# Kernel optimization log

Measured on AMD Instinct MI355X. Metric: run time of the kernel, lower is better.

## Reference

```python
import jax, jax.numpy as jnp
import numpy as np
from jax import lax

# Conv4d decomposed (as in the torch implementation) into a sum of Conv3d's
# over the first spatial kernel axis. Each 3D conv is vectorized by folding
# the strided first-dim slices into the batch dimension.

def conv4d(x, w, b, stride=(2, 2, 2, 2), padding=(1, 1, 1, 1)):
    # x: [B, Ci, D1, D2, D3, D4]; w: [Co, Ci, K1, K2, K3, K4]; b: [Co]
    B, Ci, D1, D2, D3, D4 = x.shape
    Co, _, K1, K2, K3, K4 = w.shape
    s1, p1 = stride[0], padding[0]
    T = (D1 + 2 * p1 - K1) // s1 + 1  # output size along first spatial dim
    xp = jnp.pad(x, ((0, 0), (0, 0), (p1, p1), (0, 0), (0, 0), (0, 0)))
    pad3 = [(padding[j], padding[j]) for j in (1, 2, 3)]
    out = None
    for i in range(K1):  # small fixed loop over kernel taps along dim0
        xi = xp[:, :, i:i + s1 * (T - 1) + 1:s1]           # [B, Ci, T, D2, D3, D4]
        xi = jnp.moveaxis(xi, 2, 1).reshape(B * T, Ci, D2, D3, D4)
        yi = lax.conv_general_dilated(
            xi, w[:, :, i], window_strides=stride[1:], padding=pad3,
            dimension_numbers=('NCDHW', 'OIDHW', 'NCDHW'))
        out = yi if out is None else out + yi
    O2, O3, O4 = out.shape[2], out.shape[3], out.shape[4]
    out = out.reshape(B, T, Co, O2, O3, O4)
    out = jnp.moveaxis(out, 1, 2)                          # [B, Co, T, O2, O3, O4]
    return out + b[None, :, None, None, None, None]


def setup_inputs() -> dict:
    key = jax.random.key(0)
    k0, k1, k2, k3, k4 = jax.random.split(key, 5)
    C, R = 16, 4  # in_channel, mlp_ratio
    H = C * R     # 64
    x = jax.random.normal(k0, (1, C, 32, 32, 32, 32), dtype=jnp.float32)
    w1 = jax.random.normal(k1, (H, C, 3, 3, 3, 3), dtype=jnp.float32) * 0.02
    b1 = jax.random.normal(k2, (H,), dtype=jnp.float32) * 0.02
    w2 = jax.random.normal(k3, (C, H, 3, 3, 3, 3), dtype=jnp.float32) * 0.02
    b2 = jax.random.normal(k4, (C,), dtype=jnp.float32) * 0.02
    return {'x': x, 'w1': w1, 'b1': b1, 'w2': w2, 'b2': b2}


def reference(x, w1, b1, w2, b2):
    h = conv4d(x, w1, b1)                      # [1, 64, 16, 16, 16, 16]
    h = jax.nn.gelu(h, approximate=False)      # exact erf GELU (torch default)
    return conv4d(h, w2, b2)                   # [1, 16, 8, 8, 8, 8]
```

## Files before the change

kernel.cpp:

```cpp
#include <hip/hip_runtime.h>
#include <hip/hip_bf16.h>
#include <math.h>


typedef __attribute__((ext_vector_type(8))) short short8;
typedef __attribute__((ext_vector_type(4))) float f32x4;
typedef __attribute__((ext_vector_type(4))) unsigned int uint4v;

__device__ __forceinline__ unsigned short f2bf(float v) {
    __hip_bfloat16 b = __float2bfloat16(v);
    return *(unsigned short*)&b;
}

__global__ void setup_kernel(const float* __restrict__ w1, const float* __restrict__ w2,
                             const float* __restrict__ b2,
                             unsigned short* __restrict__ w1p, unsigned short* __restrict__ w2p,
                             uint4v* __restrict__ hz, float* __restrict__ out) {
    int b = blockIdx.x, tid = threadIdx.x;
    if (b < 544) {
        int i = b * 256 + tid;
        int kp = i % 136, co = (i / 136) & 63, ci = i / 8704;
        float v = 0.f;
        if (kp < 108 && (kp & 3) < 3) v = w1[(co * 16 + ci) * 81 + (kp >> 2) * 3 + (kp & 3)];
        w1p[i] = f2bf(v);
    } else if (b < 1088) {
        int i = (b - 544) * 256 + tid;
        int kp = i % 136, co = (i / 136) & 15, ci = i / 2176;
        float v = 0.f;
        if (kp < 108 && (kp & 3) < 3) v = w2[(co * 64 + ci) * 81 + (kp >> 2) * 3 + (kp & 3)];
        w2p[i] = f2bf(v);
    } else if (b < 1344) {
        int i = (b - 1088) * 256 + tid;
        out[i] = b2[i >> 12];
    } else {
        int i = (b - 1344) * 256 + tid;
        hz[i] = (uint4v){0, 0, 0, 0};
        int j = i + 704512;
        if (j < 839808) hz[j] = (uint4v){0, 0, 0, 0};
    }
}

__global__ __launch_bounds__(256) void conv1_mfma(
        const float* __restrict__ x, const unsigned short* __restrict__ w1p,
        const float* __restrict__ b1, unsigned short* __restrict__ hpad) {
    __shared__ unsigned short sX[36000];

    const int tid = threadIdx.x;
    const int bid = blockIdx.x;
    const int t4 = bid & 1, t3 = (bid >> 1) & 7, t2 = (bid >> 4) & 7, t1 = bid >> 7;
    const int bo1 = 2 * t1, bo2 = 2 * t2, bo3 = 2 * t3, bo4 = 8 * t4;
    const int g1b = 2 * bo1 - 1, g2b = 2 * bo2 - 1, g3b = 2 * bo3 - 1, g4b = 2 * bo4 - 1;

    int offs[5], swb[5];
    unsigned mka = 0, mkb = 0;
#pragma unroll
    for (int r = 0; r < 5; ++r) {
        int u = tid + 256 * r;
        bool uok = u < 1125;
        int uu = uok ? u : 0;
        int p = uu % 9, q = uu / 9;
        int i3 = q % 5; q /= 5;
        int i2 = q % 5; int i1 = q / 5;
        int g1 = g1b + i1, g2 = g2b + i2, g3 = g3b + i3;
        bool ok123 = uok & ((unsigned)g1 < 32u) & ((unsigned)g2 < 32u) & ((unsigned)g3 < 32u);
        int g4a = g4b + 2 * p;
        offs[r] = ((g1 * 32 + g2) * 32 + g3) * 32 + g4a;
        if (ok123 && (unsigned)g4a < 32u) mka |= 1u << r;
        if (ok123 && (unsigned)(g4a + 1) < 32u) mkb |= 1u << r;
        swb[r] = 2 * (((i1 * 5 + i2) * 5 + i3) * 18 + 2 * p);
    }

    auto gatherX = [&](int ci, float (&a)[5], float (&b)[5]) {
        const float* xc = x + (size_t)ci * 1048576;
#pragma unroll
        for (int r = 0; r < 5; ++r) {
            float va = 0.f, vb = 0.f;
            if ((mka >> r) & 1) va = xc[offs[r]];
            if ((mkb >> r) & 1) vb = xc[offs[r] + 1];
            a[r] = va; b[r] = vb;
        }
    };
    auto writeSlab = [&](int ci, const float (&a)[5], const float (&b)[5]) {
        char* slab = (char*)sX + ci * 4500;
#pragma unroll
        for (int r = 0; r < 4; ++r)
            *(unsigned*)(slab + swb[r]) = (unsigned)f2bf(a[r]) | ((unsigned)f2bf(b[r]) << 16);
        if (tid < 101)
            *(unsigned*)(slab + swb[4]) = (unsigned)f2bf(a[4]) | ((unsigned)f2bf(b[4]) << 16);
    };

    {
        float a0[5], b0[5], a1[5], b1v[5];
        gatherX(0, a0, b0);
        gatherX(1, a1, b1v);
        for (int cc = 0; cc < 16; cc += 2) {
            writeSlab(cc, a0, b0);
            if (cc + 2 < 16) gatherX(cc + 2, a0, b0);
            writeSlab(cc + 1, a1, b1v);
            if (cc + 3 < 16) gatherX(cc + 3, a1, b1v);
        }
    }
    __syncthreads();

    const int lane = tid & 63, wv = tid >> 6;
    const int n16 = lane & 15, hi = lane >> 4;
    const int ct0 = 2 * (wv & 1);
    const int st0 = 2 * (wv >> 1);

    int fpb[2];
#pragma unroll
    for (int tt = 0; tt < 2; ++tt) {
        int sp = (st0 + tt) * 16 + n16;
        int o4l = sp & 7, o3l = (sp >> 3) & 1, o2l = (sp >> 4) & 1, o1l = sp >> 5;
        fpb[tt] = 2 * (900 * o1l + 180 * o2l + 36 * o3l + 2 * o4l);
    }
    int kof[4][2];
#pragma unroll
    for (int ks = 0; ks < 4; ++ks)
#pragma unroll
    for (int j = 0; j < 2; ++j) {
        int g = 8 * ks + 2 * hi + j;
        if (g > 26) g = 26;
        int k1 = g / 9, k2 = (g / 3) % 3, k3 = g % 3;
        kof[ks][j] = 2 * (450 * k1 + 90 * k2 + 18 * k3);
    }

    auto loadA = [&](int ci, short8 (&Ac)[8]) {
        const unsigned short* aw0 = w1p + (size_t)(ci * 64 + 16 * ct0 + n16) * 136 + hi * 8;
#pragma unroll
        for (int k = 0; k < 4; ++k) Ac[k] = *(const short8*)(aw0 + 32 * k);
        const unsigned short* aw1 = aw0 + 16 * 136;
#pragma unroll
        for (int k = 0; k < 4; ++k) Ac[4 + k] = *(const short8*)(aw1 + 32 * k);
    };
    auto readFR = [&](int ci, short8 (&fr)[2][4]) {
        const char* sx = (const char*)sX + ci * 4500;
#pragma unroll
        for (int tt = 0; tt < 2; ++tt) {
            const char* base = sx + fpb[tt];
#pragma unroll
            for (int ks = 0; ks < 4; ++ks) {
                unsigned r0 = *(const unsigned*)(base + kof[ks][0]);
                unsigned r1 = *(const unsigned*)(base + kof[ks][0] + 4);
                unsigned r2 = *(const unsigned*)(base + kof[ks][1]);
                unsigned r3 = *(const unsigned*)(base + kof[ks][1] + 4);
                uint4v t = (uint4v){r0, r1, r2, r3};
                fr[tt][ks] = *(short8*)&t;
            }
        }
    };

    f32x4 acc[2][2];
#pragma unroll
    for (int c = 0; c < 2; ++c)
#pragma unroll
    for (int t = 0; t < 2; ++t) acc[c][t] = (f32x4){0.f, 0.f, 0.f, 0.f};

    auto mfma16 = [&](const short8 (&Ac)[8], const short8 (&fr)[2][4]) {
        __builtin_amdgcn_s_setprio(1);
#pragma unroll
        for (int tt = 0; tt < 2; ++tt)
#pragma unroll
        for (int ks = 0; ks < 4; ++ks) {
            acc[0][tt] = __builtin_amdgcn_mfma_f32_16x16x32_bf16(Ac[ks],     fr[tt][ks], acc[0][tt], 0, 0, 0);
            acc[1][tt] = __builtin_amdgcn_mfma_f32_16x16x32_bf16(Ac[4 + ks], fr[tt][ks], acc[1][tt], 0, 0, 0);
        }
        __builtin_amdgcn_s_setprio(0);
    };

    short8 A0[8], A1[8], F0[2][4], F1[2][4];
    loadA(0, A0);
    loadA(1, A1);
    readFR(0, F0);

    for (int cc = 0; cc < 16; cc += 2) {
        readFR(cc + 1, F1);
        mfma16(A0, F0);
        if (cc < 14) { loadA(cc + 2, A0); readFR(cc + 2, F0); }
        mfma16(A1, F1);
        if (cc < 14) loadA(cc + 3, A1);
    }

#pragma unroll
    for (int c = 0; c < 2; ++c) {
#pragma unroll
        for (int tt = 0; tt < 2; ++tt) {
            int spl = 16 * (st0 + tt) + n16;
            int e4 = spl & 7, e3 = (spl >> 3) & 1, e2 = (spl >> 4) & 1, e1 = spl >> 5;
            size_t base = (size_t)(bo1 + e1 + 1) * 5832 + (bo2 + e2 + 1) * 324 +
                          (bo3 + e3 + 1) * 18 + (bo4 + e4 + 1);
#pragma unroll
            for (int r = 0; r < 4; ++r) {
                int co = 16 * (ct0 + c) + 4 * hi + r;
                float v = acc[c][tt][r] + b1[co];
                v = 0.5f * v * (1.f + erff(v * 0.70710678118654752f));
                hpad[(size_t)co * 104976 + base] = f2bf(v);
            }
        }
    }
}

__global__ __launch_bounds__(256) void conv2_mfma(
        const unsigned short* __restrict__ hpad, const unsigned short* __restrict__ w2p,
        float* __restrict__ out) {
    __shared__ unsigned short sX[18000];

    const int tid = threadIdx.x;
    const int bid = blockIdx.x;
    const int s = bid & 63, cig = bid >> 6;
    const int t3 = s & 3, t2 = (s >> 2) & 3, t1 = s >> 4;
    const int bo1 = 2 * t1, bo2 = 2 * t2, bo3 = 2 * t3;

    int offs[5], swb[5];
#pragma unroll
    for (int r = 0; r < 5; ++r) {
        int u = tid + 256 * r;
        if (u >= 1125) u = 0;
        int p = u % 9, q = u / 9;
        int i3 = q % 5; q /= 5;
        int i2 = q % 5; int i1 = q / 5;
        offs[r] = (2 * bo1 + i1) * 5832 + (2 * bo2 + i2) * 324 + (2 * bo3 + i3) * 18 + 2 * p;
        swb[r] = 2 * (((i1 * 5 + i2) * 5 + i3) * 18 + 2 * p);
    }

    {
        unsigned fa[5], na[5];
        const unsigned short* h0 = hpad + (size_t)(cig * 8) * 104976;
#pragma unroll
        for (int r = 0; r < 5; ++r) fa[r] = *(const unsigned*)(h0 + offs[r]);
        for (int s8 = 0; s8 < 8; ++s8) {
            if (s8 < 7) {
                const unsigned short* hc = hpad + (size_t)(cig * 8 + s8 + 1) * 104976;
#pragma unroll
                for (int r = 0; r < 5; ++r) na[r] = *(const unsigned*)(hc + offs[r]);
            }
            char* slab = (char*)sX + s8 * 4500;
#pragma unroll
            for (int r = 0; r < 4; ++r) *(unsigned*)(slab + swb[r]) = fa[r];
            if (tid < 101) *(unsigned*)(slab + swb[4]) = fa[4];
            if (s8 < 7) {
#pragma unroll
                for (int r = 0; r < 5; ++r) fa[r] = na[r];
            }
        }
    }
    __syncthreads();

    const int lane = tid & 63, wv = tid >> 6;
    const int n16 = lane & 15, hi = lane >> 4;

    int fpb;
    {
        int sp = wv * 16 + n16;
        int o4l = sp & 7, o3l = (sp >> 3) & 1, o2l = (sp >> 4) & 1, o1l = sp >> 5;
        fpb = 2 * (900 * o1l + 180 * o2l + 36 * o3l + 2 * o4l);
    }
    int kof[4][2];
#pragma unroll
    for (int ks = 0; ks < 4; ++ks)
#pragma unroll
    for (int j = 0; j < 2; ++j) {
        int g = 8 * ks + 2 * hi + j;
        if (g > 26) g = 26;
        int k1 = g / 9, k2 = (g / 3) % 3, k3 = g % 3;
        kof[ks][j] = 2 * (450 * k1 + 90 * k2 + 18 * k3);
    }

    auto loadA = [&](int s8, short8 (&Ac)[4]) {
        const unsigned short* aw = w2p + (size_t)((cig * 8 + s8) * 16 + n16) * 136 + hi * 8;
#pragma unroll
        for (int k = 0; k < 4; ++k) Ac[k] = *(const short8*)(aw + 32 * k);
    };
    auto readFR = [&](int s8, short8 (&fr)[4]) {
        const char* base = (const char*)sX + s8 * 4500 + fpb;
#pragma unroll
        for (int ks = 0; ks < 4; ++ks) {
            unsigned r0 = *(const unsigned*)(base + kof[ks][0]);
            unsigned r1 = *(const unsigned*)(base + kof[ks][0] + 4);
            unsigned r2 = *(const unsigned*)(base + kof[ks][1]);
            unsigned r3 = *(const unsigned*)(base + kof[ks][1] + 4);
            uint4v tmp = (uint4v){r0, r1, r2, r3};
            fr[ks] = *(short8*)&tmp;
        }
    };

    f32x4 acc = (f32x4){0.f, 0.f, 0.f, 0.f};
    short8 A0[4], A1[4], F0[4], F1[4];
    loadA(0, A0);
    loadA(1, A1);
    readFR(0, F0);

    auto mfma4 = [&](const short8 (&Ac)[4], const short8 (&fr)[4]) {
        __builtin_amdgcn_s_setprio(1);
#pragma unroll
        for (int ks = 0; ks < 4; ++ks)
            acc = __builtin_amdgcn_mfma_f32_16x16x32_bf16(Ac[ks], fr[ks], acc, 0, 0, 0);
        __builtin_amdgcn_s_setprio(0);
    };

    for (int cc = 0; cc < 8; cc += 2) {
        readFR(cc + 1, F1);
        mfma4(A0, F0);
        if (cc < 6) { loadA(cc + 2, A0); readFR(cc + 2, F0); }
        mfma4(A1, F1);
        if (cc < 6) loadA(cc + 3, A1);
    }

    {
        int spl = 16 * wv + n16;
        int e4 = spl & 7, e3 = (spl >> 3) & 1, e2 = (spl >> 4) & 1, e1 = spl >> 5;
        int o1 = bo1 + e1, o2 = bo2 + e2, o3 = bo3 + e3, o4 = e4;
#pragma unroll
        for (int r = 0; r < 4; ++r) {
            int co = 4 * hi + r;
            atomicAdd(&out[(size_t)co * 4096 + o1 * 512 + o2 * 64 + o3 * 8 + o4], acc[r]);
        }
    }
}

extern "C" void kernel_launch(void* const* d_in, const int* in_sizes, int n_in,
                              void* d_out, int out_size, void* d_ws, size_t ws_size,
                              hipStream_t stream) {
    const float* x  = (const float*)d_in[0];
    const float* w1 = (const float*)d_in[1];
    const float* b1 = (const float*)d_in[2];
    const float* w2 = (const float*)d_in[3];
    const float* b2 = (const float*)d_in[4];
    float* out = (float*)d_out;

    unsigned short* hpad = (unsigned short*)d_ws;
    unsigned short* w1p  = hpad + 6718464;
    unsigned short* w2p  = w1p + 139264;

    setup_kernel<<<4096, 256, 0, stream>>>(w1, w2, b2, w1p, w2p, (uint4v*)hpad, out);
    conv1_mfma<<<1024, 256, 0, stream>>>(x, w1p, b1, hpad);
    conv2_mfma<<<512, 256, 0, stream>>>(hpad, w2p, out);
}
```

Before: 85.98 us.

## Split conv1 tiles across eight waves and vectorize input gather

conv1_mfma now runs 512 threads per block. Each of the 8 waves computes one 16-wide spatial tile for two channel tiles, where before each of 4 waves computed two spatial tiles. The input gather fetches each pair of adjacent floats with one 8-byte load from a clamped offset, then masks the out-of-bounds values to zero, in 3 rounds instead of 5. This aims to raise wave-level parallelism and latency hiding while using fewer, wider loads. The cost is that each wave now reloads the same weight fragments, so weight traffic doubles.

```diff
diff --git a/kernel.cpp b/kernel.cpp
--- a/kernel.cpp
+++ b/kernel.cpp
@@ -6,6 +6,7 @@
 typedef __attribute__((ext_vector_type(8))) short short8;
 typedef __attribute__((ext_vector_type(4))) float f32x4;
 typedef __attribute__((ext_vector_type(4))) unsigned int uint4v;
+typedef unsigned uint2a __attribute__((ext_vector_type(2), aligned(4)));
 
 __device__ __forceinline__ unsigned short f2bf(float v) {
     __hip_bfloat16 b = __float2bfloat16(v);
@@ -40,7 +41,7 @@
     }
 }
 
-__global__ __launch_bounds__(256) void conv1_mfma(
+__global__ __launch_bounds__(512) void conv1_mfma(
         const float* __restrict__ x, const unsigned short* __restrict__ w1p,
         const float* __restrict__ b1, unsigned short* __restrict__ hpad) {
     __shared__ unsigned short sX[36000];
@@ -51,11 +52,11 @@
     const int bo1 = 2 * t1, bo2 = 2 * t2, bo3 = 2 * t3, bo4 = 8 * t4;
     const int g1b = 2 * bo1 - 1, g2b = 2 * bo2 - 1, g3b = 2 * bo3 - 1, g4b = 2 * bo4 - 1;
 
-    int offs[5], swb[5];
+    int offc[3], swb[3];
     unsigned mka = 0, mkb = 0;
 #pragma unroll
-    for (int r = 0; r < 5; ++r) {
-        int u = tid + 256 * r;
+    for (int r = 0; r < 3; ++r) {
+        int u = tid + 512 * r;
         bool uok = u < 1125;
         int uu = uok ? u : 0;
         int p = uu % 9, q = uu / 9;
@@ -64,33 +65,33 @@
         int g1 = g1b + i1, g2 = g2b + i2, g3 = g3b + i3;
         bool ok123 = uok & ((unsigned)g1 < 32u) & ((unsigned)g2 < 32u) & ((unsigned)g3 < 32u);
         int g4a = g4b + 2 * p;
-        offs[r] = ((g1 * 32 + g2) * 32 + g3) * 32 + g4a;
+        int off = ((g1 * 32 + g2) * 32 + g3) * 32 + g4a;
         if (ok123 && (unsigned)g4a < 32u) mka |= 1u << r;
         if (ok123 && (unsigned)(g4a + 1) < 32u) mkb |= 1u << r;
+        offc[r] = off < 0 ? 0 : (off > 1048574 ? 1048574 : off);
         swb[r] = 2 * (((i1 * 5 + i2) * 5 + i3) * 18 + 2 * p);
     }
 
-    auto gatherX = [&](int ci, float (&a)[5], float (&b)[5]) {
+    auto gatherX = [&](int ci, float (&a)[3], float (&b)[3]) {
         const float* xc = x + (size_t)ci * 1048576;
 #pragma unroll
-        for (int r = 0; r < 5; ++r) {
-            float va = 0.f, vb = 0.f;
-            if ((mka >> r) & 1) va = xc[offs[r]];
-            if ((mkb >> r) & 1) vb = xc[offs[r] + 1];
-            a[r] = va; b[r] = vb;
-        }
-    };
-    auto writeSlab = [&](int ci, const float (&a)[5], const float (&b)[5]) {
+        for (int r = 0; r < 3; ++r) {
+            uint2a v = *(const uint2a*)(xc + offc[r]);
+            a[r] = ((mka >> r) & 1) ? __uint_as_float(v.x) : 0.f;
+            b[r] = ((mkb >> r) & 1) ? __uint_as_float(v.y) : 0.f;
+        }
+    };
+    auto writeSlab = [&](int ci, const float (&a)[3], const float (&b)[3]) {
         char* slab = (char*)sX + ci * 4500;
 #pragma unroll
-        for (int r = 0; r < 4; ++r)
+        for (int r = 0; r < 2; ++r)
             *(unsigned*)(slab + swb[r]) = (unsigned)f2bf(a[r]) | ((unsigned)f2bf(b[r]) << 16);
         if (tid < 101)
-            *(unsigned*)(slab + swb[4]) = (unsigned)f2bf(a[4]) | ((unsigned)f2bf(b[4]) << 16);
-    };
-
-    {
-        float a0[5], b0[5], a1[5], b1v[5];
+            *(unsigned*)(slab + swb[2]) = (unsigned)f2bf(a[2]) | ((unsigned)f2bf(b[2]) << 16);
+    };
+
+    {
+        float a0[3], b0[3], a1[3], b1v[3];
         gatherX(0, a0, b0);
         gatherX(1, a1, b1v);
         for (int cc = 0; cc < 16; cc += 2) {
@@ -102,18 +103,13 @@
     }
     __syncthreads();
 
-    const int lane = tid & 63, wv = tid >> 6;
+    const int lane = tid & 63, wvv = tid >> 6;
     const int n16 = lane & 15, hi = lane >> 4;
-    const int ct0 = 2 * (wv & 1);
-    const int st0 = 2 * (wv >> 1);
-
-    int fpb[2];
-#pragma unroll
-    for (int tt = 0; tt < 2; ++tt) {
-        int sp = (st0 + tt) * 16 + n16;
-        int o4l = sp & 7, o3l = (sp >> 3) & 1, o2l = (sp >> 4) & 1, o1l = sp >> 5;
-        fpb[tt] = 2 * (900 * o1l + 180 * o2l + 36 * o3l + 2 * o4l);
-    }
+    const int stile = wvv & 3;
+    const int ct0 = 2 * (wvv >> 2);
+
+    const int fpb = 2 * (900 * (stile >> 1) + 180 * (stile & 1) +
+                         36 * ((n16 >> 3) & 1) + 2 * (n16 & 7));
     int kof[4][2];
 #pragma unroll
     for (int ks = 0; ks < 4; ++ks)
@@ -133,66 +129,57 @@
 #pragma unroll
         for (int k = 0; k < 4; ++k) Ac[4 + k] = *(const short8*)(aw1 + 32 * k);
     };
-    auto readFR = [&](int ci, short8 (&fr)[2][4]) {
-        const char* sx = (const char*)sX + ci * 4500;
-#pragma unroll
-        for (int tt = 0; tt < 2; ++tt) {
-            const char* base = sx + fpb[tt];
-#pragma unroll
-            for (int ks = 0; ks < 4; ++ks) {
-                unsigned r0 = *(const unsigned*)(base + kof[ks][0]);
-                unsigned r1 = *(const unsigned*)(base + kof[ks][0] + 4);
-                unsigned r2 = *(const unsigned*)(base + kof[ks][1]);
-                unsigned r3 = *(const unsigned*)(base + kof[ks][1] + 4);
-                uint4v t = (uint4v){r0, r1, r2, r3};
-                fr[tt][ks] = *(short8*)&t;
-            }
-        }
-    };
-
-    f32x4 acc[2][2];
-#pragma unroll
-    for (int c = 0; c < 2; ++c)
-#pragma unroll
-    for (int t = 0; t < 2; ++t) acc[c][t] = (f32x4){0.f, 0.f, 0.f, 0.f};
-
-    auto mfma16 = [&](const short8 (&Ac)[8], const short8 (&fr)[2][4]) {
+    auto readFR = [&](int ci, short8 (&fr)[4]) {
+        const char* base = (const char*)sX + ci * 4500 + fpb;
+#pragma unroll
+        for (int ks = 0; ks < 4; ++ks) {
+            unsigned r0 = *(const unsigned*)(base + kof[ks][0]);
+            unsigned r1 = *(const unsigned*)(base + kof[ks][0] + 4);
+            unsigned r2 = *(const unsigned*)(base + kof[ks][1]);
+            unsigned r3 = *(const unsigned*)(base + kof[ks][1] + 4);
+            uint4v t = (uint4v){r0, r1, r2, r3};
+            fr[ks] = *(short8*)&t;
+        }
+    };
+
+    f32x4 acc[2];
+    acc[0] = (f32x4){0.f, 0.f, 0.f, 0.f};
+    acc[1] = (f32x4){0.f, 0.f, 0.f, 0.f};
+
+    auto mfma8 = [&](const short8 (&Ac)[8], const short8 (&fr)[4]) {
         __builtin_amdgcn_s_setprio(1);
 #pragma unroll
-        for (int tt = 0; tt < 2; ++tt)
-#pragma unroll
         for (int ks = 0; ks < 4; ++ks) {
-            acc[0][tt] = __builtin_amdgcn_mfma_f32_16x16x32_bf16(Ac[ks],     fr[tt][ks], acc[0][tt], 0, 0, 0);
-            acc[1][tt] = __builtin_amdgcn_mfma_f32_16x16x32_bf16(Ac[4 + ks], fr[tt][ks], acc[1][tt], 0, 0, 0);
+            acc[0] = __builtin_amdgcn_mfma_f32_16x16x32_bf16(Ac[ks],     fr[ks], acc[0], 0, 0, 0);
+            acc[1] = __builtin_amdgcn_mfma_f32_16x16x32_bf16(Ac[4 + ks], fr[ks], acc[1], 0, 0, 0);
         }
         __builtin_amdgcn_s_setprio(0);
     };
 
-    short8 A0[8], A1[8], F0[2][4], F1[2][4];
+    short8 A0[8], A1[8], F0[4], F1[4];
     loadA(0, A0);
     loadA(1, A1);
     readFR(0, F0);
 
     for (int cc = 0; cc < 16; cc += 2) {
         readFR(cc + 1, F1);
-        mfma16(A0, F0);
+        mfma8(A0, F0);
         if (cc < 14) { loadA(cc + 2, A0); readFR(cc + 2, F0); }
-        mfma16(A1, F1);
+        mfma8(A1, F1);
         if (cc < 14) loadA(cc + 3, A1);
     }
 
-#pragma unroll
-    for (int c = 0; c < 2; ++c) {
-#pragma unroll
-        for (int tt = 0; tt < 2; ++tt) {
-            int spl = 16 * (st0 + tt) + n16;
-            int e4 = spl & 7, e3 = (spl >> 3) & 1, e2 = (spl >> 4) & 1, e1 = spl >> 5;
-            size_t base = (size_t)(bo1 + e1 + 1) * 5832 + (bo2 + e2 + 1) * 324 +
-                          (bo3 + e3 + 1) * 18 + (bo4 + e4 + 1);
+    {
+        int spl = 16 * stile + n16;
+        int e4 = spl & 7, e3 = (spl >> 3) & 1, e2 = (spl >> 4) & 1, e1 = spl >> 5;
+        size_t base = (size_t)(bo1 + e1 + 1) * 5832 + (bo2 + e2 + 1) * 324 +
+                      (bo3 + e3 + 1) * 18 + (bo4 + e4 + 1);
+#pragma unroll
+        for (int c = 0; c < 2; ++c) {
 #pragma unroll
             for (int r = 0; r < 4; ++r) {
                 int co = 16 * (ct0 + c) + 4 * hi + r;
-                float v = acc[c][tt][r] + b1[co];
+                float v = acc[c][r] + b1[co];
                 v = 0.5f * v * (1.f + erff(v * 0.70710678118654752f));
                 hpad[(size_t)co * 104976 + base] = f2bf(v);
             }
@@ -333,6 +320,6 @@
     unsigned short* w2p  = w1p + 139264;
 
     setup_kernel<<<4096, 256, 0, stream>>>(w1, w2, b2, w1p, w2p, (uint4v*)hpad, out);
-    conv1_mfma<<<1024, 256, 0, stream>>>(x, w1p, b1, hpad);
+    conv1_mfma<<<1024, 512, 0, stream>>>(x, w1p, b1, hpad);
     conv2_mfma<<<512, 256, 0, stream>>>(hpad, w2p, out);
 }
```

Measured after the change: 115.5 us. 1.34x slower.

## Halve conv1 shared-memory slab by staging input channels in two phases

Applied to the files above, without the earlier changes.

The conv1 kernel now stages only 8 input-channel slabs in LDS at a time instead of all 16, halving shared memory per block. It loads channels 0-7 and runs their MFMAs, then loads channels 8-15 into the same buffer and runs the rest, with an extra barrier in between. The aim is to fit more blocks per CU (higher occupancy) so global gathers can overlap with other blocks' compute. The cost is an extra synchronization and a serialized second load phase inside each block.

```diff
diff --git a/kernel.cpp b/kernel.cpp
--- a/kernel.cpp
+++ b/kernel.cpp
@@ -43,7 +43,7 @@
 __global__ __launch_bounds__(256) void conv1_mfma(
         const float* __restrict__ x, const unsigned short* __restrict__ w1p,
         const float* __restrict__ b1, unsigned short* __restrict__ hpad) {
-    __shared__ unsigned short sX[36000];
+    __shared__ unsigned short sX[18000];
 
     const int tid = threadIdx.x;
     const int bid = blockIdx.x;
@@ -80,27 +80,14 @@
             a[r] = va; b[r] = vb;
         }
     };
-    auto writeSlab = [&](int ci, const float (&a)[5], const float (&b)[5]) {
-        char* slab = (char*)sX + ci * 4500;
+    auto writeSlab = [&](int slot, const float (&a)[5], const float (&b)[5]) {
+        char* slab = (char*)sX + slot * 4500;
 #pragma unroll
         for (int r = 0; r < 4; ++r)
             *(unsigned*)(slab + swb[r]) = (unsigned)f2bf(a[r]) | ((unsigned)f2bf(b[r]) << 16);
         if (tid < 101)
             *(unsigned*)(slab + swb[4]) = (unsigned)f2bf(a[4]) | ((unsigned)f2bf(b[4]) << 16);
     };
-
-    {
-        float a0[5], b0[5], a1[5], b1v[5];
-        gatherX(0, a0, b0);
-        gatherX(1, a1, b1v);
-        for (int cc = 0; cc < 16; cc += 2) {
-            writeSlab(cc, a0, b0);
-            if (cc + 2 < 16) gatherX(cc + 2, a0, b0);
-            writeSlab(cc + 1, a1, b1v);
-            if (cc + 3 < 16) gatherX(cc + 3, a1, b1v);
-        }
-    }
-    __syncthreads();
 
     const int lane = tid & 63, wv = tid >> 6;
     const int n16 = lane & 15, hi = lane >> 4;
@@ -133,8 +120,8 @@
 #pragma unroll
         for (int k = 0; k < 4; ++k) Ac[4 + k] = *(const short8*)(aw1 + 32 * k);
     };
-    auto readFR = [&](int ci, short8 (&fr)[2][4]) {
-        const char* sx = (const char*)sX + ci * 4500;
+    auto readFR = [&](int slot, short8 (&fr)[2][4]) {
+        const char* sx = (const char*)sX + slot * 4500;
 #pragma unroll
         for (int tt = 0; tt < 2; ++tt) {
             const char* base = sx + fpb[tt];
@@ -169,16 +156,49 @@
     };
 
     short8 A0[8], A1[8], F0[2][4], F1[2][4];
+    float a0[5], b0[5], a1[5], b1v[5];
+
     loadA(0, A0);
     loadA(1, A1);
+
+    gatherX(0, a0, b0);
+    gatherX(1, a1, b1v);
+    for (int cc = 0; cc < 8; cc += 2) {
+        writeSlab(cc, a0, b0);
+        if (cc + 2 < 8) gatherX(cc + 2, a0, b0);
+        writeSlab(cc + 1, a1, b1v);
+        if (cc + 3 < 8) gatherX(cc + 3, a1, b1v);
+    }
+    __syncthreads();
+
     readFR(0, F0);
-
-    for (int cc = 0; cc < 16; cc += 2) {
-        readFR(cc + 1, F1);
+    for (int s = 0; s < 8; s += 2) {
+        readFR(s + 1, F1);
         mfma16(A0, F0);
-        if (cc < 14) { loadA(cc + 2, A0); readFR(cc + 2, F0); }
+        loadA(s + 2, A0);
+        if (s < 6) readFR(s + 2, F0);
         mfma16(A1, F1);
-        if (cc < 14) loadA(cc + 3, A1);
+        loadA(s + 3, A1);
+    }
+
+    gatherX(8, a0, b0);
+    gatherX(9, a1, b1v);
+    __syncthreads();
+    for (int cc = 0; cc < 8; cc += 2) {
+        writeSlab(cc, a0, b0);
+        if (cc + 2 < 8) gatherX(cc + 10, a0, b0);
+        writeSlab(cc + 1, a1, b1v);
+        if (cc + 3 < 8) gatherX(cc + 11, a1, b1v);
+    }
+    __syncthreads();
+
+    readFR(0, F0);
+    for (int s = 0; s < 8; s += 2) {
+        readFR(s + 1, F1);
+        mfma16(A0, F0);
+        if (s < 6) { loadA(s + 10, A0); readFR(s + 2, F0); }
+        mfma16(A1, F1);
+        if (s < 6) loadA(s + 11, A1);
     }
 
 #pragma unroll
```

Result: slower. 131.6 us, median of 2 (+53.0%).

## Vectorize conv1 input gather and deepen weight/fragment prefetch pipeline

Applied to the files above, without the earlier changes.

The input gather in conv1 now does one 8-byte load per pair instead of two predicated scalar loads. Offsets are clamped and the right element is selected with shift masks, so the loads need no branches. Weight loads for the first two channels are hoisted ahead of the slab gather and barrier, and the MFMA loop is deepened to four stages of A and fragment buffers. The aim is to cut global load instruction count and hide weight and LDS latency, at the cost of higher register pressure and possible occupancy loss.

```diff
diff --git a/kernel.cpp b/kernel.cpp
--- a/kernel.cpp
+++ b/kernel.cpp
@@ -6,6 +6,7 @@
 typedef __attribute__((ext_vector_type(8))) short short8;
 typedef __attribute__((ext_vector_type(4))) float f32x4;
 typedef __attribute__((ext_vector_type(4))) unsigned int uint4v;
+typedef unsigned uint2a __attribute__((ext_vector_type(2), aligned(4)));
 
 __device__ __forceinline__ unsigned short f2bf(float v) {
     __hip_bfloat16 b = __float2bfloat16(v);
@@ -51,8 +52,8 @@
     const int bo1 = 2 * t1, bo2 = 2 * t2, bo3 = 2 * t3, bo4 = 8 * t4;
     const int g1b = 2 * bo1 - 1, g2b = 2 * bo2 - 1, g3b = 2 * bo3 - 1, g4b = 2 * bo4 - 1;
 
-    int offs[5], swb[5];
-    unsigned mka = 0, mkb = 0;
+    int offc[5], swb[5];
+    unsigned mka = 0, mkb = 0, sA = 0, sB = 0;
 #pragma unroll
     for (int r = 0; r < 5; ++r) {
         int u = tid + 256 * r;
@@ -64,9 +65,13 @@
         int g1 = g1b + i1, g2 = g2b + i2, g3 = g3b + i3;
         bool ok123 = uok & ((unsigned)g1 < 32u) & ((unsigned)g2 < 32u) & ((unsigned)g3 < 32u);
         int g4a = g4b + 2 * p;
-        offs[r] = ((g1 * 32 + g2) * 32 + g3) * 32 + g4a;
+        int o = ((g1 * 32 + g2) * 32 + g3) * 32 + g4a;
         if (ok123 && (unsigned)g4a < 32u) mka |= 1u << r;
         if (ok123 && (unsigned)(g4a + 1) < 32u) mkb |= 1u << r;
+        int oc = o < 0 ? 0 : (o > 1048574 ? 1048574 : o);
+        if (o > oc) sA |= 1u << r;
+        if (o < oc) sB |= 1u << r;
+        offc[r] = oc;
         swb[r] = 2 * (((i1 * 5 + i2) * 5 + i3) * 18 + 2 * p);
     }
 
@@ -74,10 +79,12 @@
         const float* xc = x + (size_t)ci * 1048576;
 #pragma unroll
         for (int r = 0; r < 5; ++r) {
-            float va = 0.f, vb = 0.f;
-            if ((mka >> r) & 1) va = xc[offs[r]];
-            if ((mkb >> r) & 1) vb = xc[offs[r] + 1];
-            a[r] = va; b[r] = vb;
+            uint2a v = *(const uint2a*)(xc + offc[r]);
+            float lo = __uint_as_float(v.x), hiv = __uint_as_float(v.y);
+            float va = ((sA >> r) & 1) ? hiv : lo;
+            float vb = ((sB >> r) & 1) ? lo : hiv;
+            a[r] = ((mka >> r) & 1) ? va : 0.f;
+            b[r] = ((mkb >> r) & 1) ? vb : 0.f;
         }
     };
     auto writeSlab = [&](int ci, const float (&a)[5], const float (&b)[5]) {
@@ -88,6 +95,78 @@
         if (tid < 101)
             *(unsigned*)(slab + swb[4]) = (unsigned)f2bf(a[4]) | ((unsigned)f2bf(b[4]) << 16);
     };
+
+    const int lane = tid & 63, wv = tid >> 6;
+    const int n16 = lane & 15, hi = lane >> 4;
+    const int ct0 = 2 * (wv & 1);
+    const int st0 = 2 * (wv >> 1);
+
+    int fpb[2];
+#pragma unroll
+    for (int tt = 0; tt < 2; ++tt) {
+        int sp = (st0 + tt) * 16 + n16;
+        int o4l = sp & 7, o3l = (sp >> 3) & 1, o2l = (sp >> 4) & 1, o1l = sp >> 5;
+        fpb[tt] = 2 * (900 * o1l + 180 * o2l + 36 * o3l + 2 * o4l);
+    }
+    int kof[4][2];
+#pragma unroll
+    for (int ks = 0; ks < 4; ++ks)
+#pragma unroll
+    for (int j = 0; j < 2; ++j) {
+        int g = 8 * ks + 2 * hi + j;
+        if (g > 26) g = 26;
+        int k1 = g / 9, k2 = (g / 3) % 3, k3 = g % 3;
+        kof[ks][j] = 2 * (450 * k1 + 90 * k2 + 18 * k3);
+    }
+
+    auto loadA = [&](int ci, short8 (&Ac)[8]) {
+        const unsigned short* aw0 = w1p + (size_t)(ci * 64 + 16 * ct0 + n16) * 136 + hi * 8;
+#pragma unroll
+        for (int k = 0; k < 4; ++k) Ac[k] = *(const short8*)(aw0 + 32 * k);
+        const unsigned short* aw1 = aw0 + 16 * 136;
+#pragma unroll
+        for (int k = 0; k < 4; ++k) Ac[4 + k] = *(const short8*)(aw1 + 32 * k);
+    };
+    auto readFR = [&](int ci, short8 (&fr)[2][4]) {
+        const char* sx = (const char*)sX + ci * 4500;
+#pragma unroll
+        for (int tt = 0; tt < 2; ++tt) {
+            const char* base = sx + fpb[tt];
+#pragma unroll
+            for (int ks = 0; ks < 4; ++ks) {
+                unsigned r0 = *(const unsigned*)(base + kof[ks][0]);
+                unsigned r1 = *(const unsigned*)(base + kof[ks][0] + 4);
+                unsigned r2 = *(const unsigned*)(base + kof[ks][1]);
+                unsigned r3 = *(const unsigned*)(base + kof[ks][1] + 4);
+                uint4v t = (uint4v){r0, r1, r2, r3};
+                fr[tt][ks] = *(short8*)&t;
+            }
+        }
+    };
+
+    f32x4 acc[2][2];
+#pragma unroll
+    for (int c = 0; c < 2; ++c)
+#pragma unroll
+    for (int t = 0; t < 2; ++t) acc[c][t] = (f32x4){0.f, 0.f, 0.f, 0.f};
+
+    auto mfma16 = [&](const short8 (&Ac)[8], const short8 (&fr)[2][4]) {
+        __builtin_amdgcn_s_setprio(1);
+#pragma unroll
+        for (int tt = 0; tt < 2; ++tt)
+#pragma unroll
+        for (int ks = 0; ks < 4; ++ks) {
+            acc[0][tt] = __builtin_amdgcn_mfma_f32_16x16x32_bf16(Ac[ks],     fr[tt][ks], acc[0][tt], 0, 0, 0);
+            acc[1][tt] = __builtin_amdgcn_mfma_f32_16x16x32_bf16(Ac[4 + ks], fr[tt][ks], acc[1][tt], 0, 0, 0);
+        }
+        __builtin_amdgcn_s_setprio(0);
+    };
+
+    short8 A0[8], A1[8], A2[8], A3[8];
+    short8 F0[2][4], F1[2][4], F2[2][4], F3[2][4];
+
+    loadA(0, A0);
+    loadA(1, A1);
 
     {
         float a0[5], b0[5], a1[5], b1v[5];
@@ -102,83 +181,24 @@
     }
     __syncthreads();
 
-    const int lane = tid & 63, wv = tid >> 6;
-    const int n16 = lane & 15, hi = lane >> 4;
-    const int ct0 = 2 * (wv & 1);
-    const int st0 = 2 * (wv >> 1);
-
-    int fpb[2];
-#pragma unroll
-    for (int tt = 0; tt < 2; ++tt) {
-        int sp = (st0 + tt) * 16 + n16;
-        int o4l = sp & 7, o3l = (sp >> 3) & 1, o2l = (sp >> 4) & 1, o1l = sp >> 5;
-        fpb[tt] = 2 * (900 * o1l + 180 * o2l + 36 * o3l + 2 * o4l);
-    }
-    int kof[4][2];
-#pragma unroll
-    for (int ks = 0; ks < 4; ++ks)
-#pragma unroll
-    for (int j = 0; j < 2; ++j) {
-        int g = 8 * ks + 2 * hi + j;
-        if (g > 26) g = 26;
-        int k1 = g / 9, k2 = (g / 3) % 3, k3 = g % 3;
-        kof[ks][j] = 2 * (450 * k1 + 90 * k2 + 18 * k3);
-    }
-
-    auto loadA = [&](int ci, short8 (&Ac)[8]) {
-        const unsigned short* aw0 = w1p + (size_t)(ci * 64 + 16 * ct0 + n16) * 136 + hi * 8;
-#pragma unroll
-        for (int k = 0; k < 4; ++k) Ac[k] = *(const short8*)(aw0 + 32 * k);
-        const unsigned short* aw1 = aw0 + 16 * 136;
-#pragma unroll
-        for (int k = 0; k < 4; ++k) Ac[4 + k] = *(const short8*)(aw1 + 32 * k);
-    };
-    auto readFR = [&](int ci, short8 (&fr)[2][4]) {
-        const char* sx = (const char*)sX + ci * 4500;
-#pragma unroll
-        for (int tt = 0; tt < 2; ++tt) {
-            const char* base = sx + fpb[tt];
-#pragma unroll
-            for (int ks = 0; ks < 4; ++ks) {
-                unsigned r0 = *(const unsigned*)(base + kof[ks][0]);
-                unsigned r1 = *(const unsigned*)(base + kof[ks][0] + 4);
-                unsigned r2 = *(const unsigned*)(base + kof[ks][1]);
-                unsigned r3 = *(const unsigned*)(base + kof[ks][1] + 4);
-                uint4v t = (uint4v){r0, r1, r2, r3};
-                fr[tt][ks] = *(short8*)&t;
-            }
-        }
-    };
-
-    f32x4 acc[2][2];
-#pragma unroll
-    for (int c = 0; c < 2; ++c)
-#pragma unroll
-    for (int t = 0; t < 2; ++t) acc[c][t] = (f32x4){0.f, 0.f, 0.f, 0.f};
-
-    auto mfma16 = [&](const short8 (&Ac)[8], const short8 (&fr)[2][4]) {
-        __builtin_amdgcn_s_setprio(1);
-#pragma unroll
-        for (int tt = 0; tt < 2; ++tt)
-#pragma unroll
-        for (int ks = 0; ks < 4; ++ks) {
-            acc[0][tt] = __builtin_amdgcn_mfma_f32_16x16x32_bf16(Ac[ks],     fr[tt][ks], acc[0][tt], 0, 0, 0);
-            acc[1][tt] = __builtin_amdgcn_mfma_f32_16x16x32_bf16(Ac[4 + ks], fr[tt][ks], acc[1][tt], 0, 0, 0);
-        }
-        __builtin_amdgcn_s_setprio(0);
-    };
-
-    short8 A0[8], A1[8], F0[2][4], F1[2][4];
-    loadA(0, A0);
-    loadA(1, A1);
+    loadA(2, A2);
+    loadA(3, A3);
     readFR(0, F0);
-
-    for (int cc = 0; cc < 16; cc += 2) {
-        readFR(cc + 1, F1);
+    readFR(1, F1);
+
+    for (int cc = 0; cc < 16; cc += 4) {
+        readFR(cc + 2, F2);
         mfma16(A0, F0);
-        if (cc < 14) { loadA(cc + 2, A0); readFR(cc + 2, F0); }
+        if (cc < 12) loadA(cc + 4, A0);
+        readFR(cc + 3, F3);
         mfma16(A1, F1);
-        if (cc < 14) loadA(cc + 3, A1);
+        if (cc < 12) loadA(cc + 5, A1);
+        if (cc < 12) readFR(cc + 4, F0);
+        mfma16(A2, F2);
+        if (cc < 12) loadA(cc + 6, A2);
+        if (cc < 12) readFR(cc + 5, F1);
+        mfma16(A3, F3);
+        if (cc < 12) loadA(cc + 7, A3);
     }
 
 #pragma unroll
```

After: 100.9 us. +17.3%, slower.
